# Optimization experiments

Hardware: AMD Instinct MI355X
Metric: run time of the kernel (lower is better)

The kernel has to match this reference:

```python
import jax, jax.numpy as jnp
import numpy as np

N, NPER, B, E = 65536, 1024, 64, 1048576
IN_F, HID, K, NCLS = 128, 64, 16, 10


def setup_inputs() -> dict:
    key = jax.random.key(0)
    ks = jax.random.split(key, 12)
    x = jax.random.normal(ks[0], (N, IN_F), jnp.float32)
    # block-structured intra-graph edges: 64 graphs of 1024 contiguous nodes
    gid = jax.random.randint(ks[1], (E,), 0, B)
    src = gid * NPER + jax.random.randint(ks[2], (E,), 0, NPER)
    dst = gid * NPER + jax.random.randint(ks[3], (E,), 0, NPER)
    edge_index = jnp.stack([src, dst]).astype(jnp.int32)
    batch = (jnp.arange(N, dtype=jnp.int32) // NPER).astype(jnp.int32)
    def lin(k, fo, fi):
        kw, kb = jax.random.split(k)
        s = 1.0 / np.sqrt(fi)
        return (jax.random.uniform(kw, (fo, fi), jnp.float32, -s, s),
                jax.random.uniform(kb, (fo,), jnp.float32, -s, s))
    W1, b1 = lin(ks[4], HID, IN_F)
    W2, b2 = lin(ks[5], HID, HID)
    Wp, bp = lin(ks[6], K, HID)      # DMoN cluster-assignment MLP (single Linear)
    Wl, bl = lin(ks[7], NCLS, HID)   # final classifier
    return {"x": x, "edge_index": edge_index, "batch": batch,
            "W1": W1, "b1": b1, "W2": W2, "b2": b2,
            "Wp": Wp, "bp": bp, "Wl": Wl, "bl": bl}


def gcn_conv(x, src, dst, W, b):
    # GCNConv with add_self_loops=True, symmetric normalization
    n = x.shape[0]
    deg = jax.ops.segment_sum(jnp.ones(src.shape[0], x.dtype), dst,
                              num_segments=n) + 1.0  # +1 for self-loop
    dinv = jax.lax.rsqrt(deg)
    h = x @ W.T
    coef = (dinv[src] * dinv[dst])[:, None]
    agg = jax.ops.segment_sum(h[src] * coef, dst, num_segments=n)
    agg = agg + h * (dinv * dinv)[:, None]  # self-loop contribution
    return agg + b


def reference(x, edge_index, batch, W1, b1, W2, b2, Wp, bp, Wl, bl):
    src, dst = edge_index[0], edge_index[1]
    h = jax.nn.relu(gcn_conv(x, src, dst, W1, b1))
    h = jax.nn.relu(gcn_conv(h, src, dst, W2, b2))
    # to_dense_batch: graphs are equal-sized and contiguous -> reshape, mask all True
    Xb = h.reshape(B, NPER, HID)
    # DMoN cluster assignment (dropout=0.0, mask all ones)
    s = jax.nn.softmax(Xb @ Wp.T + bp, axis=-1)          # [B, NPER, K]
    Xp = jax.nn.selu(jnp.einsum('bnk,bnh->bkh', s, Xb))   # pooled clusters [B, K, HID]
    out = Xp.mean(axis=1)                                  # [B, HID]
    logits = out @ Wl.T + bl                               # [B, NCLS]
    return logits
```

## Files before the change

kernel.cpp:

```cpp
#include <hip/hip_runtime.h>
#include <cstddef>

#define N_NODES 65536
#define NPER    1024
#define NGRAPH  64
#define HID     64
#define IN_F    128
#define KCLUS   16
#define NCLS    10
#define NCAP    64
#define HSTRIDE 12
#define LIN_BLOCKS 512

template <int K>
__device__ __forceinline__ void gemm_tile(const float* __restrict__ X,
                                          const float* __restrict__ W,
                                          float* __restrict__ Y,
                                          float (*xs)[68], float (*ws)[68],
                                          int block, int t) {
    const size_t row0 = (size_t)block * 128;
    const int rbase = t >> 3;
    const int cbase = t & 7;
    float acc[4][8] = {};

    for (int kc = 0; kc < K; kc += 64) {
        __syncthreads();
        for (int i = t; i < 128 * 16; i += 256) {
            int row = i >> 4, k4 = (i & 15) << 2;
            *(float4*)&xs[row][k4] = *(const float4*)(X + (row0 + row) * K + kc + k4);
        }
        for (int i = t; i < 64 * 16; i += 256) {
            int col = i >> 4, k4 = (i & 15) << 2;
            *(float4*)&ws[col][k4] = *(const float4*)(W + col * K + kc + k4);
        }
        __syncthreads();

#pragma unroll 4
        for (int k4 = 0; k4 < 64; k4 += 4) {
            float4 xr[4], wr[8];
#pragma unroll
            for (int rr = 0; rr < 4; ++rr) xr[rr] = *(const float4*)&xs[rbase + 32 * rr][k4];
#pragma unroll
            for (int cc = 0; cc < 8; ++cc) wr[cc] = *(const float4*)&ws[cbase + 8 * cc][k4];
#pragma unroll
            for (int rr = 0; rr < 4; ++rr)
#pragma unroll
                for (int cc = 0; cc < 8; ++cc) {
                    acc[rr][cc] = fmaf(xr[rr].x, wr[cc].x, acc[rr][cc]);
                    acc[rr][cc] = fmaf(xr[rr].y, wr[cc].y, acc[rr][cc]);
                    acc[rr][cc] = fmaf(xr[rr].z, wr[cc].z, acc[rr][cc]);
                    acc[rr][cc] = fmaf(xr[rr].w, wr[cc].w, acc[rr][cc]);
                }
        }
    }

#pragma unroll
    for (int rr = 0; rr < 4; ++rr)
#pragma unroll
        for (int cc = 0; cc < 8; ++cc)
            Y[(row0 + rbase + 32 * rr) * HID + cbase + 8 * cc] = acc[rr][cc];
}

__global__ __launch_bounds__(256) void front_kernel(const float* __restrict__ X,
                                                    const float* __restrict__ W,
                                                    float* __restrict__ Y,
                                                    const int* __restrict__ src,
                                                    const int* __restrict__ dst,
                                                    int* __restrict__ deg,
                                                    unsigned short* __restrict__ es, int E) {
    __shared__ float xs[128][68];
    __shared__ float ws[64][68];
    const int t = threadIdx.x;

    if (blockIdx.x >= LIN_BLOCKS) {
        const int e0 = (blockIdx.x - LIN_BLOCKS) * 1024;
#pragma unroll
        for (int i = 0; i < 4; ++i) {
            int idx = e0 + i * 256 + t;
            if (idx < E) {
                int d = dst[idx], s = src[idx];
                int pos = atomicAdd(&deg[d], 1);
                if (pos < NCAP) es[(size_t)d * NCAP + pos] = (unsigned short)(s & 1023);
            }
        }
        return;
    }

    gemm_tile<IN_F>(X, W, Y, xs, ws, blockIdx.x, t);
}

template <int K>
__global__ __launch_bounds__(256) void linear_kernel(const float* __restrict__ X,
                                                     const float* __restrict__ W,
                                                     float* __restrict__ Y) {
    __shared__ float xs[128][68];
    __shared__ float ws[64][68];
    gemm_tile<K>(X, W, Y, xs, ws, blockIdx.x, threadIdx.x);
}

__global__ __launch_bounds__(512) void agg_kernel(const float* __restrict__ h,
                                                  const unsigned short* __restrict__ es,
                                                  const int* __restrict__ deg,
                                                  const float* __restrict__ bias,
                                                  float* __restrict__ outp) {
    __shared__ float Hs[NPER * HSTRIDE];
    __shared__ float dl[NPER];
    const int g = blockIdx.x & 63;
    const int f0 = (blockIdx.x >> 6) * 8;
    const int t = threadIdx.x;
    const int base = g * NPER;

    for (int r = t; r < NPER; r += 512) {
        const float* hp = h + (size_t)(base + r) * HID + f0;
        float4 a = *(const float4*)hp;
        float4 b = *(const float4*)(hp + 4);
        float dv = rsqrtf((float)deg[base + r] + 1.0f);
        dl[r] = dv;
        float* row = &Hs[r * HSTRIDE];
        *(float4*)row = make_float4(a.x * dv, a.y * dv, a.z * dv, a.w * dv);
        *(float4*)(row + 4) = make_float4(b.x * dv, b.y * dv, b.z * dv, b.w * dv);
    }
    float bb[8];
#pragma unroll
    for (int j = 0; j < 8; ++j) bb[j] = bias[f0 + j];
    __syncthreads();

    for (int ld = t; ld < NPER; ld += 512) {
        const unsigned short* ep = es + (size_t)(base + ld) * NCAP;
        int dg = deg[base + ld];
        dg = dg < NCAP ? dg : NCAP;
        const float* srow = &Hs[ld * HSTRIDE];
        float4 acc0 = *(const float4*)srow;
        float4 acc1 = *(const float4*)(srow + 4);
        float4 bcc0 = make_float4(0.f, 0.f, 0.f, 0.f);
        float4 bcc1 = make_float4(0.f, 0.f, 0.f, 0.f);

        int p = 0;
        const int p4 = dg & ~3;
        for (; p < p4; p += 4) {
            uint2 w4 = *(const uint2*)(ep + p);
            const float* r0 = &Hs[(int)(w4.x & 0xFFFFu) * HSTRIDE];
            const float* r1 = &Hs[(int)(w4.x >> 16) * HSTRIDE];
            const float* r2 = &Hs[(int)(w4.y & 0xFFFFu) * HSTRIDE];
            const float* r3 = &Hs[(int)(w4.y >> 16) * HSTRIDE];
            float4 a0 = *(const float4*)r0, a1 = *(const float4*)(r0 + 4);
            float4 b0 = *(const float4*)r1, b1 = *(const float4*)(r1 + 4);
            float4 c0v = *(const float4*)r2, c1v = *(const float4*)(r2 + 4);
            float4 d0 = *(const float4*)r3, d1 = *(const float4*)(r3 + 4);
            acc0.x += a0.x; acc0.y += a0.y; acc0.z += a0.z; acc0.w += a0.w;
            acc1.x += a1.x; acc1.y += a1.y; acc1.z += a1.z; acc1.w += a1.w;
            bcc0.x += b0.x; bcc0.y += b0.y; bcc0.z += b0.z; bcc0.w += b0.w;
            bcc1.x += b1.x; bcc1.y += b1.y; bcc1.z += b1.z; bcc1.w += b1.w;
            acc0.x += c0v.x; acc0.y += c0v.y; acc0.z += c0v.z; acc0.w += c0v.w;
            acc1.x += c1v.x; acc1.y += c1v.y; acc1.z += c1v.z; acc1.w += c1v.w;
            bcc0.x += d0.x; bcc0.y += d0.y; bcc0.z += d0.z; bcc0.w += d0.w;
            bcc1.x += d1.x; bcc1.y += d1.y; bcc1.z += d1.z; bcc1.w += d1.w;
        }
        for (; p < dg; ++p) {
            const float* rr = &Hs[(int)ep[p] * HSTRIDE];
            float4 e0 = *(const float4*)rr, e1 = *(const float4*)(rr + 4);
            acc0.x += e0.x; acc0.y += e0.y; acc0.z += e0.z; acc0.w += e0.w;
            acc1.x += e1.x; acc1.y += e1.y; acc1.z += e1.z; acc1.w += e1.w;
        }
        acc0.x += bcc0.x; acc0.y += bcc0.y; acc0.z += bcc0.z; acc0.w += bcc0.w;
        acc1.x += bcc1.x; acc1.y += bcc1.y; acc1.z += bcc1.z; acc1.w += bcc1.w;

        const float dv = dl[ld];
        float4 o0, o1;
        o0.x = fmaxf(fmaf(acc0.x, dv, bb[0]), 0.f);
        o0.y = fmaxf(fmaf(acc0.y, dv, bb[1]), 0.f);
        o0.z = fmaxf(fmaf(acc0.z, dv, bb[2]), 0.f);
        o0.w = fmaxf(fmaf(acc0.w, dv, bb[3]), 0.f);
        o1.x = fmaxf(fmaf(acc1.x, dv, bb[4]), 0.f);
        o1.y = fmaxf(fmaf(acc1.y, dv, bb[5]), 0.f);
        o1.z = fmaxf(fmaf(acc1.z, dv, bb[6]), 0.f);
        o1.w = fmaxf(fmaf(acc1.w, dv, bb[7]), 0.f);
        float* op = outp + (size_t)(base + ld) * HID + f0;
        *(float4*)op = o0;
        *(float4*)(op + 4) = o1;
    }
}

__global__ __launch_bounds__(256) void pool1_kernel(const float* __restrict__ h,
                                                    const float* __restrict__ Wp,
                                                    const float* __restrict__ bp,
                                                    float* __restrict__ xpart) {
    __shared__ float xs[128][HID + 1];
    __shared__ float ss[128][KCLUS + 1];
    __shared__ float wp[KCLUS][HID];
    __shared__ float bps[KCLUS];
    const int g = blockIdx.x >> 3;
    const int c = blockIdx.x & 7;
    const int t = threadIdx.x;
    const float* hb = h + ((size_t)g * NPER + c * 128) * HID;

    for (int i = t; i < 128 * HID / 4; i += 256) {
        float4 v = ((const float4*)hb)[i];
        int row = i >> 4, col = (i & 15) * 4;
        xs[row][col] = v.x; xs[row][col + 1] = v.y; xs[row][col + 2] = v.z; xs[row][col + 3] = v.w;
    }
    for (int i = t; i < KCLUS * HID; i += 256) wp[i >> 6][i & 63] = Wp[i];
    if (t < KCLUS) bps[t] = bp[t];
    __syncthreads();

    if (t < 128) {
        float lg[KCLUS];
        float mx = -1e30f;
#pragma unroll
        for (int k = 0; k < KCLUS; ++k) {
            float a = bps[k];
#pragma unroll 8
            for (int hh = 0; hh < HID; ++hh) a = fmaf(xs[t][hh], wp[k][hh], a);
            lg[k] = a;
            mx = fmaxf(mx, a);
        }
        float sum = 0.f;
#pragma unroll
        for (int k = 0; k < KCLUS; ++k) {
            lg[k] = __expf(lg[k] - mx);
            sum += lg[k];
        }
        float inv = 1.0f / sum;
#pragma unroll
        for (int k = 0; k < KCLUS; ++k) ss[t][k] = lg[k] * inv;
    }
    __syncthreads();

    const int hcol = t & 63;
    const int k0 = (t >> 6) * 4;
    float a0 = 0.f, a1 = 0.f, a2 = 0.f, a3 = 0.f;
#pragma unroll 8
    for (int n = 0; n < 128; ++n) {
        float xv = xs[n][hcol];
        a0 = fmaf(ss[n][k0 + 0], xv, a0);
        a1 = fmaf(ss[n][k0 + 1], xv, a1);
        a2 = fmaf(ss[n][k0 + 2], xv, a2);
        a3 = fmaf(ss[n][k0 + 3], xv, a3);
    }
    float* xp = xpart + (((size_t)(g * 8 + c)) * KCLUS + k0) * HID + hcol;
    xp[0] = a0; xp[HID] = a1; xp[2 * HID] = a2; xp[3 * HID] = a3;
}

__global__ __launch_bounds__(256) void pool2_kernel(const float* __restrict__ xpart,
                                                    const float* __restrict__ Wl,
                                                    const float* __restrict__ bl,
                                                    float* __restrict__ out) {
    __shared__ float xp[KCLUS][HID + 1];
    __shared__ float outm[HID];
    const int g = blockIdx.x;
    const int t = threadIdx.x;
    const int hcol = t & 63;
    const int k0 = (t >> 6) * 4;
    const float* base = xpart + (size_t)g * 8 * KCLUS * HID;

    float a[4] = {};
#pragma unroll
    for (int c = 0; c < 8; ++c)
#pragma unroll
        for (int j = 0; j < 4; ++j)
            a[j] += base[(c * KCLUS + k0 + j) * HID + hcol];

    const float sc = 1.0507009873554805f, al = 1.6732632423543772f;
#pragma unroll
    for (int j = 0; j < 4; ++j) {
        float v = a[j];
        xp[k0 + j][hcol] = v > 0.f ? sc * v : sc * al * (__expf(v) - 1.f);
    }
    __syncthreads();

    if (t < HID) {
        float m = 0.f;
#pragma unroll
        for (int k = 0; k < KCLUS; ++k) m += xp[k][t];
        outm[t] = m * (1.0f / KCLUS);
    }
    __syncthreads();

    if (t < NCLS) {
        float acc = bl[t];
#pragma unroll 8
        for (int hh = 0; hh < HID; ++hh) acc = fmaf(outm[hh], Wl[t * HID + hh], acc);
        out[g * NCLS + t] = acc;
    }
}

extern "C" void kernel_launch(void* const* d_in, const int* in_sizes, int n_in,
                              void* d_out, int out_size, void* d_ws, size_t ws_size,
                              hipStream_t stream) {
    const float* x  = (const float*)d_in[0];
    const int* eidx = (const int*)d_in[1];
    const float* W1 = (const float*)d_in[3];
    const float* b1 = (const float*)d_in[4];
    const float* W2 = (const float*)d_in[5];
    const float* b2 = (const float*)d_in[6];
    const float* Wp = (const float*)d_in[7];
    const float* bp = (const float*)d_in[8];
    const float* Wl = (const float*)d_in[9];
    const float* bl = (const float*)d_in[10];
    float* out = (float*)d_out;

    const int E = in_sizes[1] / 2;
    const int* src = eidx;
    const int* dst = eidx + E;

    char* w = (char*)d_ws;
    int*            deg   = (int*)w;            w += (size_t)N_NODES * 4;
    unsigned short* es    = (unsigned short*)w; w += (size_t)N_NODES * NCAP * 2;
    float*          A     = (float*)w;          w += (size_t)N_NODES * HID * 4;
    float*          Bf    = (float*)w;          w += (size_t)N_NODES * HID * 4;
    float*          xpart = (float*)w;          w += (size_t)NGRAPH * 8 * KCLUS * HID * 4;

    hipMemsetAsync(deg, 0, (size_t)N_NODES * 4, stream);

    const int nbuild = (E + 1023) / 1024;
    front_kernel<<<LIN_BLOCKS + nbuild, 256, 0, stream>>>(x, W1, A, src, dst, deg, es, E);

    agg_kernel<<<NGRAPH * 8, 512, 0, stream>>>(A, es, deg, b1, Bf);

    linear_kernel<HID><<<N_NODES / 128, 256, 0, stream>>>(Bf, W2, A);
    agg_kernel<<<NGRAPH * 8, 512, 0, stream>>>(A, es, deg, b2, Bf);

    pool1_kernel<<<NGRAPH * 8, 256, 0, stream>>>(Bf, Wp, bp, xpart);
    pool2_kernel<<<NGRAPH, 256, 0, stream>>>(xpart, Wl, bl, out);
}
```

Baseline: 227.0 us.

## Interleave edge lists into planes and fuse pooling into one per-graph kernel

The per-node neighbor list is stored in planes of four entries, so adjacent nodes' index quads sit next to each other and agg reads them coalesced. The scalar remainder loop becomes a single quad load with predicated adds. The two pooling kernels are merged into one 1024-thread block per graph that loops over eight 128-node chunks, removing the xpart round trip and one launch. The cost is only 64 blocks for pooling, with most threads idle during the softmax and accumulation phases.

```diff
diff --git a/kernel.cpp b/kernel.cpp
--- a/kernel.cpp
+++ b/kernel.cpp
@@ -9,6 +9,7 @@
 #define KCLUS   16
 #define NCLS    10
 #define NCAP    64
+#define PLANE   (N_NODES * 4)
 #define HSTRIDE 12
 #define LIN_BLOCKS 512
 
@@ -80,7 +81,9 @@
             if (idx < E) {
                 int d = dst[idx], s = src[idx];
                 int pos = atomicAdd(&deg[d], 1);
-                if (pos < NCAP) es[(size_t)d * NCAP + pos] = (unsigned short)(s & 1023);
+                if (pos < NCAP)
+                    es[(size_t)(pos >> 2) * PLANE + (size_t)d * 4 + (pos & 3)] =
+                        (unsigned short)(s & 1023);
             }
         }
         return;
@@ -126,7 +129,6 @@
     __syncthreads();
 
     for (int ld = t; ld < NPER; ld += 512) {
-        const unsigned short* ep = es + (size_t)(base + ld) * NCAP;
         int dg = deg[base + ld];
         dg = dg < NCAP ? dg : NCAP;
         const float* srow = &Hs[ld * HSTRIDE];
@@ -135,10 +137,10 @@
         float4 bcc0 = make_float4(0.f, 0.f, 0.f, 0.f);
         float4 bcc1 = make_float4(0.f, 0.f, 0.f, 0.f);
 
-        int p = 0;
-        const int p4 = dg & ~3;
-        for (; p < p4; p += 4) {
-            uint2 w4 = *(const uint2*)(ep + p);
+        const unsigned short* ep = es + (size_t)(base + ld) * 4;
+        const int nq = dg >> 2, rem = dg & 3;
+        for (int q = 0; q < nq; ++q) {
+            uint2 w4 = *(const uint2*)(ep + (size_t)q * PLANE);
             const float* r0 = &Hs[(int)(w4.x & 0xFFFFu) * HSTRIDE];
             const float* r1 = &Hs[(int)(w4.x >> 16) * HSTRIDE];
             const float* r2 = &Hs[(int)(w4.y & 0xFFFFu) * HSTRIDE];
@@ -156,11 +158,27 @@
             bcc0.x += d0.x; bcc0.y += d0.y; bcc0.z += d0.z; bcc0.w += d0.w;
             bcc1.x += d1.x; bcc1.y += d1.y; bcc1.z += d1.z; bcc1.w += d1.w;
         }
-        for (; p < dg; ++p) {
-            const float* rr = &Hs[(int)ep[p] * HSTRIDE];
-            float4 e0 = *(const float4*)rr, e1 = *(const float4*)(rr + 4);
-            acc0.x += e0.x; acc0.y += e0.y; acc0.z += e0.z; acc0.w += e0.w;
-            acc1.x += e1.x; acc1.y += e1.y; acc1.z += e1.z; acc1.w += e1.w;
+        if (rem) {
+            uint2 w4 = *(const uint2*)(ep + (size_t)nq * PLANE);
+            unsigned sx0 = w4.x & 0xFFFFu, sx1 = w4.x >> 16, sx2 = w4.y & 0xFFFFu;
+            {
+                const float* rr = &Hs[(int)sx0 * HSTRIDE];
+                float4 e0 = *(const float4*)rr, e1 = *(const float4*)(rr + 4);
+                acc0.x += e0.x; acc0.y += e0.y; acc0.z += e0.z; acc0.w += e0.w;
+                acc1.x += e1.x; acc1.y += e1.y; acc1.z += e1.z; acc1.w += e1.w;
+            }
+            if (rem > 1) {
+                const float* rr = &Hs[(int)sx1 * HSTRIDE];
+                float4 e0 = *(const float4*)rr, e1 = *(const float4*)(rr + 4);
+                bcc0.x += e0.x; bcc0.y += e0.y; bcc0.z += e0.z; bcc0.w += e0.w;
+                bcc1.x += e1.x; bcc1.y += e1.y; bcc1.z += e1.z; bcc1.w += e1.w;
+            }
+            if (rem > 2) {
+                const float* rr = &Hs[(int)sx2 * HSTRIDE];
+                float4 e0 = *(const float4*)rr, e1 = *(const float4*)(rr + 4);
+                acc0.x += e0.x; acc0.y += e0.y; acc0.z += e0.z; acc0.w += e0.w;
+                acc1.x += e1.x; acc1.y += e1.y; acc1.z += e1.z; acc1.w += e1.w;
+            }
         }
         acc0.x += bcc0.x; acc0.y += bcc0.y; acc0.z += bcc0.z; acc0.w += bcc0.w;
         acc1.x += bcc1.x; acc1.y += bcc1.y; acc1.z += bcc1.z; acc1.w += bcc1.w;
@@ -181,90 +199,81 @@
     }
 }
 
-__global__ __launch_bounds__(256) void pool1_kernel(const float* __restrict__ h,
-                                                    const float* __restrict__ Wp,
-                                                    const float* __restrict__ bp,
-                                                    float* __restrict__ xpart) {
+__global__ __launch_bounds__(1024) void megapool_kernel(const float* __restrict__ h,
+                                                        const float* __restrict__ Wp,
+                                                        const float* __restrict__ bp,
+                                                        const float* __restrict__ Wl,
+                                                        const float* __restrict__ bl,
+                                                        float* __restrict__ out) {
     __shared__ float xs[128][HID + 1];
     __shared__ float ss[128][KCLUS + 1];
     __shared__ float wp[KCLUS][HID];
     __shared__ float bps[KCLUS];
-    const int g = blockIdx.x >> 3;
-    const int c = blockIdx.x & 7;
-    const int t = threadIdx.x;
-    const float* hb = h + ((size_t)g * NPER + c * 128) * HID;
-
-    for (int i = t; i < 128 * HID / 4; i += 256) {
-        float4 v = ((const float4*)hb)[i];
-        int row = i >> 4, col = (i & 15) * 4;
-        xs[row][col] = v.x; xs[row][col + 1] = v.y; xs[row][col + 2] = v.z; xs[row][col + 3] = v.w;
-    }
-    for (int i = t; i < KCLUS * HID; i += 256) wp[i >> 6][i & 63] = Wp[i];
-    if (t < KCLUS) bps[t] = bp[t];
-    __syncthreads();
-
-    if (t < 128) {
-        float lg[KCLUS];
-        float mx = -1e30f;
-#pragma unroll
-        for (int k = 0; k < KCLUS; ++k) {
-            float a = bps[k];
-#pragma unroll 8
-            for (int hh = 0; hh < HID; ++hh) a = fmaf(xs[t][hh], wp[k][hh], a);
-            lg[k] = a;
-            mx = fmaxf(mx, a);
-        }
-        float sum = 0.f;
-#pragma unroll
-        for (int k = 0; k < KCLUS; ++k) {
-            lg[k] = __expf(lg[k] - mx);
-            sum += lg[k];
-        }
-        float inv = 1.0f / sum;
-#pragma unroll
-        for (int k = 0; k < KCLUS; ++k) ss[t][k] = lg[k] * inv;
-    }
-    __syncthreads();
-
-    const int hcol = t & 63;
-    const int k0 = (t >> 6) * 4;
-    float a0 = 0.f, a1 = 0.f, a2 = 0.f, a3 = 0.f;
-#pragma unroll 8
-    for (int n = 0; n < 128; ++n) {
-        float xv = xs[n][hcol];
-        a0 = fmaf(ss[n][k0 + 0], xv, a0);
-        a1 = fmaf(ss[n][k0 + 1], xv, a1);
-        a2 = fmaf(ss[n][k0 + 2], xv, a2);
-        a3 = fmaf(ss[n][k0 + 3], xv, a3);
-    }
-    float* xp = xpart + (((size_t)(g * 8 + c)) * KCLUS + k0) * HID + hcol;
-    xp[0] = a0; xp[HID] = a1; xp[2 * HID] = a2; xp[3 * HID] = a3;
-}
-
-__global__ __launch_bounds__(256) void pool2_kernel(const float* __restrict__ xpart,
-                                                    const float* __restrict__ Wl,
-                                                    const float* __restrict__ bl,
-                                                    float* __restrict__ out) {
     __shared__ float xp[KCLUS][HID + 1];
     __shared__ float outm[HID];
     const int g = blockIdx.x;
     const int t = threadIdx.x;
     const int hcol = t & 63;
-    const int k0 = (t >> 6) * 4;
-    const float* base = xpart + (size_t)g * 8 * KCLUS * HID;
-
-    float a[4] = {};
-#pragma unroll
-    for (int c = 0; c < 8; ++c)
-#pragma unroll
-        for (int j = 0; j < 4; ++j)
-            a[j] += base[(c * KCLUS + k0 + j) * HID + hcol];
-
-    const float sc = 1.0507009873554805f, al = 1.6732632423543772f;
-#pragma unroll
-    for (int j = 0; j < 4; ++j) {
-        float v = a[j];
-        xp[k0 + j][hcol] = v > 0.f ? sc * v : sc * al * (__expf(v) - 1.f);
+    const int k0 = ((t >> 6) & 3) * 4;
+
+    for (int i = t; i < KCLUS * HID; i += 1024) wp[i >> 6][i & 63] = Wp[i];
+    if (t < KCLUS) bps[t] = bp[t];
+
+    float acc4[4] = {0.f, 0.f, 0.f, 0.f};
+
+    for (int c = 0; c < 8; ++c) {
+        __syncthreads();
+        const float* hb = h + ((size_t)g * NPER + c * 128) * HID;
+        for (int i = t; i < 128 * HID / 4; i += 1024) {
+            float4 v = ((const float4*)hb)[i];
+            int row = i >> 4, col = (i & 15) * 4;
+            xs[row][col] = v.x; xs[row][col + 1] = v.y;
+            xs[row][col + 2] = v.z; xs[row][col + 3] = v.w;
+        }
+        __syncthreads();
+
+        if (t < 128) {
+            float lg[KCLUS];
+            float mx = -1e30f;
+#pragma unroll
+            for (int k = 0; k < KCLUS; ++k) {
+                float a = bps[k];
+#pragma unroll 8
+                for (int hh = 0; hh < HID; ++hh) a = fmaf(xs[t][hh], wp[k][hh], a);
+                lg[k] = a;
+                mx = fmaxf(mx, a);
+            }
+            float sum = 0.f;
+#pragma unroll
+            for (int k = 0; k < KCLUS; ++k) {
+                lg[k] = __expf(lg[k] - mx);
+                sum += lg[k];
+            }
+            float inv = 1.0f / sum;
+#pragma unroll
+            for (int k = 0; k < KCLUS; ++k) ss[t][k] = lg[k] * inv;
+        }
+        __syncthreads();
+
+        if (t < 256) {
+#pragma unroll 8
+            for (int n = 0; n < 128; ++n) {
+                float xv = xs[n][hcol];
+                acc4[0] = fmaf(ss[n][k0 + 0], xv, acc4[0]);
+                acc4[1] = fmaf(ss[n][k0 + 1], xv, acc4[1]);
+                acc4[2] = fmaf(ss[n][k0 + 2], xv, acc4[2]);
+                acc4[3] = fmaf(ss[n][k0 + 3], xv, acc4[3]);
+            }
+        }
+    }
+
+    if (t < 256) {
+        const float sc = 1.0507009873554805f, al = 1.6732632423543772f;
+#pragma unroll
+        for (int j = 0; j < 4; ++j) {
+            float v = acc4[j];
+            xp[k0 + j][hcol] = v > 0.f ? sc * v : sc * al * (__expf(v) - 1.f);
+        }
     }
     __syncthreads();
 
@@ -304,11 +313,10 @@
     const int* dst = eidx + E;
 
     char* w = (char*)d_ws;
-    int*            deg   = (int*)w;            w += (size_t)N_NODES * 4;
-    unsigned short* es    = (unsigned short*)w; w += (size_t)N_NODES * NCAP * 2;
-    float*          A     = (float*)w;          w += (size_t)N_NODES * HID * 4;
-    float*          Bf    = (float*)w;          w += (size_t)N_NODES * HID * 4;
-    float*          xpart = (float*)w;          w += (size_t)NGRAPH * 8 * KCLUS * HID * 4;
+    int*            deg = (int*)w;            w += (size_t)N_NODES * 4;
+    unsigned short* es  = (unsigned short*)w; w += (size_t)N_NODES * NCAP * 2;
+    float*          A   = (float*)w;          w += (size_t)N_NODES * HID * 4;
+    float*          Bf  = (float*)w;          w += (size_t)N_NODES * HID * 4;
 
     hipMemsetAsync(deg, 0, (size_t)N_NODES * 4, stream);
 
@@ -320,6 +328,5 @@
     linear_kernel<HID><<<N_NODES / 128, 256, 0, stream>>>(Bf, W2, A);
     agg_kernel<<<NGRAPH * 8, 512, 0, stream>>>(A, es, deg, b2, Bf);
 
-    pool1_kernel<<<NGRAPH * 8, 256, 0, stream>>>(Bf, Wp, bp, xpart);
-    pool2_kernel<<<NGRAPH, 256, 0, stream>>>(xpart, Wl, bl, out);
-}
+    megapool_kernel<<<NGRAPH, 1024, 0, stream>>>(Bf, Wp, bp, Wl, bl, out);
+}
```

After: 306.7 us. 35.1% more time.
